# Performance work log

Measured on AMD Instinct MI355X. Metric: run time of the kernel, lower is better.

## Reference

```python
import jax, jax.numpy as jnp
import numpy as np

B, CIN, COUT = 16, 32, 64
H = W = 64
K = 3                      # kernel side
GRID_SIZE, SPLINE_ORDER = 5, 3
P = K * K                  # in_features of each KANLinear
GR0, GR1 = -1.0, 1.0       # grid_range


def make_grid():
    # torch: grid = arange(-k, G+k+1)*h + grid_range[0], expanded to (in_features, G+2k+1)
    h = (GR1 - GR0) / GRID_SIZE
    g = jnp.arange(-SPLINE_ORDER, GRID_SIZE + SPLINE_ORDER + 1, dtype=jnp.float32) * h + GR0
    return jnp.broadcast_to(g, (P, g.shape[0]))


def b_splines(x, grid):
    # Cox-de Boor recursion. x: (..., P) -> bases: (..., P, GRID_SIZE+SPLINE_ORDER)
    xe = x[..., None]
    bases = ((xe >= grid[:, :-1]) & (xe < grid[:, 1:])).astype(x.dtype)
    for j in range(1, SPLINE_ORDER + 1):
        left = (xe - grid[:, : -(j + 1)]) / (grid[:, j:-1] - grid[:, : -(j + 1)])
        right = (grid[:, j + 1 :] - xe) / (grid[:, j + 1 :] - grid[:, 1:-j])
        bases = left * bases[..., :-1] + right * bases[..., 1:]
    return bases


def setup_inputs() -> dict:
    key = jax.random.key(0)
    k1, k2, k3, k4 = jax.random.split(key, 4)
    x = jax.random.normal(k1, (B, CIN, H, W), dtype=jnp.float32)
    base_weight = jax.random.normal(k2, (COUT, CIN, P), dtype=jnp.float32) * (1.0 / np.sqrt(P))
    spline_weight = jax.random.normal(k3, (COUT, CIN, P, GRID_SIZE + SPLINE_ORDER), dtype=jnp.float32) * 0.1
    spline_scaler = jax.random.normal(k4, (COUT, CIN, P), dtype=jnp.float32) * (1.0 / np.sqrt(P))
    return {"x": x, "base_weight": base_weight, "spline_weight": spline_weight, "spline_scaler": spline_scaler}


def reference(x, base_weight, spline_weight, spline_scaler):
    grid = make_grid()
    # im2col like torch.nn.Unfold: (B, CIN*P, Hout, Wout), channel-major feature order
    patches = jax.lax.conv_general_dilated_patches(x, (K, K), (1, 1), "VALID")
    _, _, Ho, Wo = patches.shape
    patches = patches.reshape(B, CIN, P, Ho * Wo).transpose(0, 1, 3, 2)  # (B, CIN, L, P)
    # base branch: SiLU(x) @ base_weight^T, summed over input channels per output channel
    base_out = jnp.einsum("bclp,ocp->bol", jax.nn.silu(patches), base_weight)
    # spline branch: B-spline bases contracted with scaled spline weights
    bases = b_splines(patches, grid)                       # (B, CIN, L, P, G+k)
    scaled_w = spline_weight * spline_scaler[..., None]    # (COUT, CIN, P, G+k)
    spline_out = jnp.einsum("bclpg,ocpg->bol", bases, scaled_w)
    return (base_out + spline_out).reshape(B, COUT, Ho, Wo)
```

## Files before the change

### kernel.cpp

```cpp
#include <hip/hip_runtime.h>


typedef short v8s __attribute__((ext_vector_type(8)));
typedef float v4f __attribute__((ext_vector_type(4)));
typedef int   v4i __attribute__((ext_vector_type(4)));
typedef int   v8i __attribute__((ext_vector_type(8)));

#define WMX_OFF     20972032u
#define WF8_OFF     21103104u
#define WPACKS_OFF  21119488u

#define SCALE1 0x7F7F7F7Fu

__device__ __forceinline__ unsigned short f2bf(float f) {
  unsigned int u = __float_as_uint(f);
  u += 0x7fffu + ((u >> 16) & 1u);
  return (unsigned short)(u >> 16);
}

__global__ __launch_bounds__(256) void k_wpack(const float* __restrict__ bw,
                                               const float* __restrict__ sw,
                                               const float* __restrict__ sc,
                                               unsigned char* __restrict__ ws) {
  int tid = blockIdx.x * 256 + threadIdx.x;
  if (tid >= 165888) return;
  if (tid < 147456) {
    int k, dst;
    if (tid < 131072) {
      int bh = tid & 15, lane = (tid >> 4) & 63, pc = (tid >> 10) & 1;
      int ss = (tid >> 13) & 1, p = tid >> 14;
      k = p * 288 + ss * 128 + (lane >> 4) * 32 + pc * 16 + bh;
      dst = WMX_OFF + tid;
    } else {
      int t2 = tid - 131072;
      int e = t2 & 7, lane = (t2 >> 3) & 63, p = t2 >> 11;
      k = p * 288 + 256 + (lane >> 4) * 8 + e;
      dst = WF8_OFF + t2;
    }
    int ot = (tid < 131072) ? ((tid >> 11) & 3) : (((tid - 131072) >> 9) & 3);
    int lane = (tid < 131072) ? ((tid >> 4) & 63) : (((tid - 131072) >> 3) & 63);
    int o = (ot << 4) + (lane & 15);
    int chunk = k / 24, u = k - chunk * 24;
    int dj = u >> 3, g = u & 7;
    int c = chunk / 3, di = chunk - c * 3;
    int p_tap = di * 3 + dj;
    float val = sw[((size_t)(o * 32 + c) * 9 + p_tap) * 8 + g] *
                sc[(size_t)(o * 32 + c) * 9 + p_tap];
    ws[dst] = (unsigned char)(__builtin_amdgcn_cvt_pk_fp8_f32(val, 0.f, 0, false) & 0xff);
  } else {
    int t2 = tid - 147456;
    int e = t2 & 7, lane = (t2 >> 3) & 63, ot = (t2 >> 9) & 3, sp = t2 >> 11;
    int o = (ot << 4) + (lane & 15);
    int cc = ((lane >> 4) << 3) + e;
    float val = bw[(size_t)(o * 32 + cc) * 9 + sp];
    *(unsigned short*)(ws + WPACKS_OFF + (size_t)t2 * 2) = f2bf(val);
  }
}

__device__ __forceinline__ void ld16(unsigned char* ldsp, const unsigned char* gp) {
  __builtin_amdgcn_global_load_lds(
      (const __attribute__((address_space(1))) unsigned int*)gp,
      (__attribute__((address_space(3))) unsigned int*)ldsp, 16, 0, 0);
}

__global__ __launch_bounds__(512) void k_gemm(const unsigned char* __restrict__ ws,
                                              const float* __restrict__ x,
                                              float* __restrict__ out) {
  __shared__ __align__(16) unsigned char wl8[2][18432];
  __shared__ __align__(16) unsigned char fl8[2][12544];
  __shared__ __align__(16) unsigned char wsil[36864];
  __shared__ __align__(16) unsigned char fsil[25088];

  const int blk = blockIdx.x;
  const int b = blk >> 4, ig = blk & 15;
  const int i0 = ig * 4;
  const int tid = threadIdx.x;
  const int wave = tid >> 6, lane = tid & 63;
  const int q = lane >> 4, ln = lane & 15;
  const int r = wave >> 1, oh = wave & 1;
  const int i = i0 + r;

  const bool factive = tid < 384;
  const int frow = tid >> 6, fx = tid & 63;
  const int fy = min(i0 + frow, 63);

  auto stage_w = [&](int p, int bi) {
#pragma unroll
    for (int it = 0; it < 3; ++it) {
      const int u = wave + it * 8;
      if (u < 16) {
        ld16(&wl8[bi][u * 1024], ws + WMX_OFF + (size_t)p * 16384 + (size_t)u * 1024 + lane * 16);
      } else if (u < 18) {
        ld16(&wl8[bi][u * 1024], ws + WF8_OFF + (size_t)p * 2048 + (size_t)(u - 16) * 1024 + lane * 16);
      }
    }
  };

  auto stage_wsil = [&]() {
#pragma unroll
    for (int it = 0; it < 5; ++it) {
      const int u = wave + it * 8;
      if (u < 36) ld16(&wsil[u * 1024], ws + WPACKS_OFF + (size_t)u * 1024 + lane * 16);
    }
  };

  auto feat_load = [&](int p, float* v) {
    if (factive) {
#pragma unroll
      for (int cp = 0; cp < 4; ++cp)
        v[cp] = x[((size_t)(b * 32 + p * 4 + cp) * 64 + fy) * 64 + fx];
    }
  };

  auto feat_store = [&](int p, int bi, const float* v) {
    if (factive) {
      unsigned long long spl[4];
      unsigned short hh[4];
#pragma unroll
      for (int cp = 0; cp < 4; ++cp) {
        const float vv = v[cp];
        hh[cp] = f2bf(vv / (1.0f + __expf(-vv)));
        float s = (vv + 2.2f) * 2.5f;
        int ii = (int)floorf(s);
        ii = ii < 0 ? 0 : (ii > 10 ? 10 : ii);
        const float uu = (vv + 2.2f) - 0.4f * (float)ii;
        float N0 = (0.4f - uu) * 2.5f;
        float N1 = uu * 2.5f;
        float a0 = N0 * 1.25f, a1 = N1 * 1.25f;
        N0 = (0.4f - uu) * a0;
        float N2 = uu * a1;
        N1 = (uu + 0.4f) * a0 + (0.8f - uu) * a1;
        float c0 = N0 * (1.0f / 1.2f), c1 = N1 * (1.0f / 1.2f), c2 = N2 * (1.0f / 1.2f);
        N0 = (0.4f - uu) * c0;
        float N3 = uu * c2;
        N1 = (uu + 0.8f) * c0 + (0.8f - uu) * c1;
        N2 = (uu + 0.4f) * c1 + (1.2f - uu) * c2;
        unsigned w0 = __builtin_amdgcn_cvt_pk_fp8_f32(N0, N1, 0, false);
        w0 = __builtin_amdgcn_cvt_pk_fp8_f32(N2, N3, w0, true);
        unsigned long long wd = w0;
        const int sh = ii * 8 - 24;
        wd = (sh >= 0) ? (wd << sh) : (wd >> (-sh));
        if (!(vv >= -2.2f && vv < 2.2f)) wd = 0;
        spl[cp] = wd;
      }
#pragma unroll
      for (int cp = 0; cp < 4; ++cp)
        *(unsigned long long*)(&fl8[bi][cp * 3072 + frow * 512 + fx * 8]) = spl[cp];
      unsigned long long sp = (unsigned long long)((unsigned)hh[0] | ((unsigned)hh[1] << 16)) |
                              ((unsigned long long)((unsigned)hh[2] | ((unsigned)hh[3] << 16)) << 32);
      *(unsigned long long*)(&fsil[frow * 4096 + fx * 64 +
                                   (((p >> 1) ^ (fx & 3)) * 16) + (p & 1) * 8]) = sp;
    }
  };

  auto offf = [&](int sg, int qq) {
    int rid = 4 * sg + qq;
    int ch = rid / 3, sub = rid - ch * 3;
    int cp = ch / 3, di = ch - cp * 3;
    return cp * 3072 + (r + di) * 512 + (sub + ln) * 8;
  };
  int offA[4], offB[4];
#pragma unroll
  for (int qq = 0; qq < 4; ++qq) { offA[qq] = offf(q, qq); offB[qq] = offf(4 + q, qq); }
  const int off8 = offf(8, q);

  v4f acc[2][4];
#pragma unroll
  for (int a = 0; a < 2; ++a)
#pragma unroll
    for (int c = 0; c < 4; ++c) acc[a][c] = (v4f){0.f, 0.f, 0.f, 0.f};

  stage_wsil();
  stage_w(0, 0);
  {
    float v0[4];
    feat_load(0, v0);
    feat_store(0, 0, v0);
  }
  __syncthreads();

#pragma unroll 1
  for (int t = 0; t < 8; ++t) {
    float vbuf[4];
    if (t < 7) {
      stage_w(t + 1, (t + 1) & 1);
      feat_load(t + 1, vbuf);
    }
    const unsigned char* wb = wl8[t & 1];
    const unsigned char* fb = fl8[t & 1];
#pragma unroll
    for (int ss = 0; ss < 2; ++ss) {
      union { v8i v; v4i h[2]; } wf[2];
#pragma unroll
      for (int tt = 0; tt < 2; ++tt) {
        const unsigned char* wp = wb + ss * 8192 + (oh * 2 + tt) * 2048 + lane * 16;
        wf[tt].h[0] = *(const v4i*)(wp);
        wf[tt].h[1] = *(const v4i*)(wp + 1024);
      }
      const int* offs = ss ? offB : offA;
      union { v8i v; long l[4]; } ff[4];
#pragma unroll
      for (int pt = 0; pt < 4; ++pt)
#pragma unroll
        for (int qq = 0; qq < 4; ++qq)
          ff[pt].l[qq] = *(const long*)(fb + offs[qq] + pt * 128);
#pragma unroll
      for (int tt = 0; tt < 2; ++tt)
#pragma unroll
        for (int pt = 0; pt < 4; ++pt)
          acc[tt][pt] = __builtin_amdgcn_mfma_scale_f32_16x16x128_f8f6f4(
              wf[tt].v, ff[pt].v, acc[tt][pt], 0, 0, 0, SCALE1, 0, SCALE1);
    }
    {
      long w8[2], f8[4];
#pragma unroll
      for (int tt = 0; tt < 2; ++tt)
        w8[tt] = *(const long*)(wb + 16384 + (oh * 2 + tt) * 512 + lane * 8);
#pragma unroll
      for (int pt = 0; pt < 4; ++pt)
        f8[pt] = *(const long*)(fb + off8 + pt * 128);
#pragma unroll
      for (int tt = 0; tt < 2; ++tt)
#pragma unroll
        for (int pt = 0; pt < 4; ++pt)
          acc[tt][pt] = __builtin_amdgcn_mfma_f32_16x16x32_fp8_fp8(
              w8[tt], f8[pt], acc[tt][pt], 0, 0, 0);
    }
    if (t < 7) feat_store(t + 1, (t + 1) & 1, vbuf);
    __syncthreads();
  }

#pragma unroll
  for (int e = 0; e < 9; ++e) {
    const int di = e / 3, dj = e % 3;
    v8s wb2[2], fb2[4];
#pragma unroll
    for (int tt = 0; tt < 2; ++tt)
      wb2[tt] = *(const v8s*)(&wsil[0] + e * 4096 + (oh * 2 + tt) * 1024 + lane * 16);
    const int xb = dj + ln;
    const int sbase = (r + di) * 4096 + xb * 64 + ((q ^ (xb & 3)) * 16);
#pragma unroll
    for (int pt = 0; pt < 4; ++pt)
      fb2[pt] = *(const v8s*)(&fsil[0] + sbase + pt * 1024);
#pragma unroll
    for (int tt = 0; tt < 2; ++tt)
#pragma unroll
      for (int pt = 0; pt < 4; ++pt)
        acc[tt][pt] = __builtin_amdgcn_mfma_f32_16x16x32_bf16(
            wb2[tt], fb2[pt], acc[tt][pt], 0, 0, 0);
  }

  if (i < 62) {
#pragma unroll
    for (int tt = 0; tt < 2; ++tt)
#pragma unroll
      for (int pt = 0; pt < 4; ++pt) {
        const int j = pt * 16 + ln;
        if (j < 62) {
#pragma unroll
          for (int rr = 0; rr < 4; ++rr) {
            const int o = (oh * 2 + tt) * 16 + q * 4 + rr;
            out[(((size_t)b * 64 + o) * 62 + i) * 62 + j] = acc[tt][pt][rr];
          }
        }
      }
  }
}

extern "C" void kernel_launch(void* const* d_in, const int* in_sizes, int n_in,
                              void* d_out, int out_size, void* d_ws, size_t ws_size,
                              hipStream_t stream) {
  const float* x  = (const float*)d_in[0];
  const float* bw = (const float*)d_in[1];
  const float* sw = (const float*)d_in[2];
  const float* sc = (const float*)d_in[3];
  unsigned char* ws = (unsigned char*)d_ws;
  float* out = (float*)d_out;

  hipLaunchKernelGGL(k_wpack, dim3(648), dim3(256), 0, stream, bw, sw, sc, ws);
  hipLaunchKernelGGL(k_gemm,  dim3(256), dim3(512), 0, stream, ws, x, out);
}
```

Before: 92.05 us.

## Vectorize weight packing and deepen feature prefetch with MFMA priority hints

The weight-packing kernel is rewritten so each thread reads one contiguous 8-float spline row, scales it, packs it to eight fp8 bytes and writes them with one 64-bit store. This replaces one-byte gathers and cuts the grid from 648 to 80 blocks. The GEMM loop now prefetches features two stages ahead in registers and stores the next stage before the MFMA work, which moves the LDS store off the tail of each iteration. It also raises wave priority around the MFMA blocks with s_setprio, at the cost of extra registers for the second prefetch buffer.

```diff
diff --git a/kernel.cpp b/kernel.cpp
--- a/kernel.cpp
+++ b/kernel.cpp
@@ -22,38 +22,48 @@
                                                const float* __restrict__ sw,
                                                const float* __restrict__ sc,
                                                unsigned char* __restrict__ ws) {
-  int tid = blockIdx.x * 256 + threadIdx.x;
-  if (tid >= 165888) return;
-  if (tid < 147456) {
-    int k, dst;
-    if (tid < 131072) {
-      int bh = tid & 15, lane = (tid >> 4) & 63, pc = (tid >> 10) & 1;
-      int ss = (tid >> 13) & 1, p = tid >> 14;
-      k = p * 288 + ss * 128 + (lane >> 4) * 32 + pc * 16 + bh;
-      dst = WMX_OFF + tid;
+  const int bid = blockIdx.x, t = threadIdx.x;
+  if (bid < 72) {
+    const int idx = bid * 256 + t;
+    const int o = idx / 288, rem = idx - o * 288;
+    const int c = rem / 9, p_tap = rem - c * 9;
+    const float scv = sc[idx];
+    const float4 v0 = *(const float4*)(sw + (size_t)idx * 8);
+    const float4 v1 = *(const float4*)(sw + (size_t)idx * 8 + 4);
+    unsigned lo = __builtin_amdgcn_cvt_pk_fp8_f32(v0.x * scv, v0.y * scv, 0, false);
+    lo = __builtin_amdgcn_cvt_pk_fp8_f32(v0.z * scv, v0.w * scv, lo, true);
+    unsigned hi = __builtin_amdgcn_cvt_pk_fp8_f32(v1.x * scv, v1.y * scv, 0, false);
+    hi = __builtin_amdgcn_cvt_pk_fp8_f32(v1.z * scv, v1.w * scv, hi, true);
+    const int di = p_tap / 3, dj = p_tap - di * 3;
+    const int k0 = 24 * (c * 3 + di) + 8 * dj;
+    const int p = k0 / 288, r288 = k0 - p * 288;
+    const int ot = o >> 4, ol = o & 15;
+    size_t dst;
+    if (r288 < 256) {
+      const int ss = r288 >> 7, r128 = r288 & 127;
+      const int lh = r128 >> 5, r32 = r128 & 31;
+      const int pc = r32 >> 4, bh = r32 & 15;
+      dst = WMX_OFF + p * 16384 + ss * 8192 + ot * 2048 + pc * 1024 +
+            (lh * 16 + ol) * 16 + bh;
     } else {
-      int t2 = tid - 131072;
-      int e = t2 & 7, lane = (t2 >> 3) & 63, p = t2 >> 11;
-      k = p * 288 + 256 + (lane >> 4) * 8 + e;
-      dst = WF8_OFF + t2;
-    }
-    int ot = (tid < 131072) ? ((tid >> 11) & 3) : (((tid - 131072) >> 9) & 3);
-    int lane = (tid < 131072) ? ((tid >> 4) & 63) : (((tid - 131072) >> 3) & 63);
-    int o = (ot << 4) + (lane & 15);
-    int chunk = k / 24, u = k - chunk * 24;
-    int dj = u >> 3, g = u & 7;
-    int c = chunk / 3, di = chunk - c * 3;
-    int p_tap = di * 3 + dj;
-    float val = sw[((size_t)(o * 32 + c) * 9 + p_tap) * 8 + g] *
-                sc[(size_t)(o * 32 + c) * 9 + p_tap];
-    ws[dst] = (unsigned char)(__builtin_amdgcn_cvt_pk_fp8_f32(val, 0.f, 0, false) & 0xff);
+      const int r2 = r288 - 256;
+      dst = WF8_OFF + p * 2048 + ot * 512 + ((r2 >> 3) * 16 + ol) * 8;
+    }
+    *(unsigned long long*)(ws + dst) =
+        (unsigned long long)lo | ((unsigned long long)hi << 32);
   } else {
-    int t2 = tid - 147456;
-    int e = t2 & 7, lane = (t2 >> 3) & 63, ot = (t2 >> 9) & 3, sp = t2 >> 11;
-    int o = (ot << 4) + (lane & 15);
-    int cc = ((lane >> 4) << 3) + e;
-    float val = bw[(size_t)(o * 32 + cc) * 9 + sp];
-    *(unsigned short*)(ws + WPACKS_OFF + (size_t)t2 * 2) = f2bf(val);
+    const int idx2 = (bid - 72) * 256 + t;
+    if (idx2 >= 2048) return;
+    const int o = idx2 >> 5, cc = idx2 & 31;
+    const int ot = o >> 4;
+    const int lane = ((cc >> 3) << 4) | (o & 15);
+    const int e = cc & 7;
+#pragma unroll
+    for (int sp = 0; sp < 9; ++sp) {
+      const float val = bw[(size_t)(o * 32 + cc) * 9 + sp];
+      *(unsigned short*)(ws + WPACKS_OFF + sp * 4096 + ot * 1024 + lane * 16 + e * 2) =
+          f2bf(val);
+    }
   }
 }
 
@@ -170,24 +180,26 @@
 #pragma unroll
     for (int c = 0; c < 4; ++c) acc[a][c] = (v4f){0.f, 0.f, 0.f, 0.f};
 
+  float v0[4], vcur[4];
+  float vnext[4] = {0.f, 0.f, 0.f, 0.f};
+  feat_load(0, v0);
+  feat_load(1, vcur);
   stage_wsil();
   stage_w(0, 0);
-  {
-    float v0[4];
-    feat_load(0, v0);
-    feat_store(0, 0, v0);
-  }
+  feat_store(0, 0, v0);
   __syncthreads();
 
 #pragma unroll 1
   for (int t = 0; t < 8; ++t) {
-    float vbuf[4];
     if (t < 7) {
+      feat_store(t + 1, (t + 1) & 1, vcur);
       stage_w(t + 1, (t + 1) & 1);
-      feat_load(t + 1, vbuf);
-    }
+    }
+    if (t < 6) feat_load(t + 2, vnext);
+
     const unsigned char* wb = wl8[t & 1];
     const unsigned char* fb = fl8[t & 1];
+    __builtin_amdgcn_s_setprio(1);
 #pragma unroll
     for (int ss = 0; ss < 2; ++ss) {
       union { v8i v; v4i h[2]; } wf[2];
@@ -226,7 +238,11 @@
           acc[tt][pt] = __builtin_amdgcn_mfma_f32_16x16x32_fp8_fp8(
               w8[tt], f8[pt], acc[tt][pt], 0, 0, 0);
     }
-    if (t < 7) feat_store(t + 1, (t + 1) & 1, vbuf);
+    __builtin_amdgcn_s_setprio(0);
+    if (t < 6) {
+#pragma unroll
+      for (int cp = 0; cp < 4; ++cp) vcur[cp] = vnext[cp];
+    }
     __syncthreads();
   }
 
@@ -242,12 +258,14 @@
 #pragma unroll
     for (int pt = 0; pt < 4; ++pt)
       fb2[pt] = *(const v8s*)(&fsil[0] + sbase + pt * 1024);
+    __builtin_amdgcn_s_setprio(1);
 #pragma unroll
     for (int tt = 0; tt < 2; ++tt)
 #pragma unroll
       for (int pt = 0; pt < 4; ++pt)
         acc[tt][pt] = __builtin_amdgcn_mfma_f32_16x16x32_bf16(
             wb2[tt], fb2[pt], acc[tt][pt], 0, 0, 0);
+    __builtin_amdgcn_s_setprio(0);
   }
 
   if (i < 62) {
@@ -277,6 +295,6 @@
   unsigned char* ws = (unsigned char*)d_ws;
   float* out = (float*)d_out;
 
-  hipLaunchKernelGGL(k_wpack, dim3(648), dim3(256), 0, stream, bw, sw, sc, ws);
+  hipLaunchKernelGGL(k_wpack, dim3(80),  dim3(256), 0, stream, bw, sw, sc, ws);
   hipLaunchKernelGGL(k_gemm,  dim3(256), dim3(512), 0, stream, ws, x, out);
 }
```

Measured after the change: 91.50 us. No clear change (-0.6%).
